# Performance work log

Measured on AMD Instinct MI355X. Metric: run time of the kernel, lower is better.

The kernel has to match this reference:

```python
import jax, jax.numpy as jnp
import numpy as np

N = 100000
E = 1600000
L = 128   # latent_size
H = 128   # hidden_size
O = 128   # output_size


def setup_inputs() -> dict:
    key = jax.random.key(0)
    ks = jax.random.split(key, 16)
    s = 1.0 / np.sqrt(H)
    inp = {
        "z": jax.random.normal(ks[0], (N, L), dtype=jnp.float32),
        "edge_index": jax.random.randint(ks[1], (2, E), 0, N, dtype=jnp.int64),
        # LSTM params (torch order: i, f, g, o)
        "W_ih": jax.random.uniform(ks[2], (4 * H, L), jnp.float32, -s, s),
        "W_hh": jax.random.uniform(ks[3], (4 * H, H), jnp.float32, -s, s),
        "b_ih": jax.random.uniform(ks[4], (4 * H,), jnp.float32, -s, s),
        "b_hh": jax.random.uniform(ks[5], (4 * H,), jnp.float32, -s, s),
        # GCNConv weights (x @ W + b)
        "W1": jax.random.uniform(ks[6], (H, H), jnp.float32, -s, s),
        "b1": jnp.zeros((H,), jnp.float32),
        "W2": jax.random.uniform(ks[7], (H, H), jnp.float32, -s, s),
        "b2": jnp.zeros((H,), jnp.float32),
        # final Linear
        "W3": jax.random.uniform(ks[8], (O, H), jnp.float32, -s, s),
        "b3": jax.random.uniform(ks[9], (O,), jnp.float32, -s, s),
    }
    return inp


def _gcn_conv(x, W, b, src, dst, norm, n_nodes):
    # x: [N, H]; src/dst/norm: [E+N] (self-loops included)
    h = x @ W                                   # [N, H] transform first (H==H)
    msg = h[src] * norm[:, None]                # gather + edge scale
    out = jax.ops.segment_sum(msg, dst, num_segments=n_nodes)  # scatter-add
    return out + b


def _lstm_step(z, W_ih, W_hh, b_ih, b_hh):
    # single time-step, h0 = c0 = 0
    gates = z @ W_ih.T + (jnp.zeros((1, H), z.dtype) @ W_hh.T) + b_ih + b_hh
    i, f, g, o = jnp.split(gates, 4, axis=-1)
    c = jax.nn.sigmoid(i) * jnp.tanh(g)         # f * c0 == 0
    return jax.nn.sigmoid(o) * jnp.tanh(c)


def reference(z, edge_index, W_ih, W_hh, b_ih, b_hh, W1, b1, W2, b2, W3, b3):
    n = z.shape[0]
    # add self-loops (PyG GCNConv default)
    loop = jnp.arange(n, dtype=edge_index.dtype)
    src = jnp.concatenate([edge_index[0], loop])
    dst = jnp.concatenate([edge_index[1], loop])
    # symmetric normalization: deg from dst (incoming, incl. self-loop)
    deg = jax.ops.segment_sum(jnp.ones_like(dst, dtype=z.dtype), dst, num_segments=n)
    dinv = jnp.where(deg > 0, jax.lax.rsqrt(deg), 0.0)
    norm = dinv[src] * dinv[dst]

    h = _lstm_step(z, W_ih, W_hh, b_ih, b_hh)
    x = jax.nn.relu(_gcn_conv(h, W1, b1, src, dst, norm, n))
    x = _gcn_conv(x, W2, b2, src, dst, norm, n)
    return jax.nn.relu(x @ W3.T + b3)
```

## Files before the change

### kernel.cpp

```cpp
#include <hip/hip_runtime.h>
#include <math.h>

typedef __attribute__((ext_vector_type(8))) short short8;
typedef __attribute__((ext_vector_type(4))) float floatx4;

#define HDIM 128
#define NPB 256
#define BKMAX 1024
#define CHUNK 8192
#define STAGE_CAP 8192

__device__ __forceinline__ float bf2f(unsigned short u) {
    unsigned int x = ((unsigned int)u) << 16;
    float f;
    __builtin_memcpy(&f, &x, 4);
    return f;
}
__device__ __forceinline__ unsigned short f2bf(float f) {
    unsigned int x;
    __builtin_memcpy(&x, &f, 4);
    unsigned int r = (x + 0x7fffu + ((x >> 16) & 1u)) >> 16;
    return (unsigned short)r;
}
__device__ __forceinline__ void split1(float v, unsigned short& hi, unsigned short& lo) {
    unsigned int x;
    __builtin_memcpy(&x, &v, 4);
    hi = (unsigned short)(x >> 16);
    lo = f2bf(v - bf2f(hi));
}
__device__ __forceinline__ float fast_sigmoid(float x) {
    return 1.0f / (1.0f + __expf(-x));
}
__device__ __forceinline__ float fast_tanh(float x) {
    float ax = fabsf(x);
    float e = __expf(2.0f * ax);
    float t = 1.0f - 2.0f / (e + 1.0f);
    return copysignf(t, x);
}

__device__ __forceinline__ void gload_lds16(const void* g, void* lds) {
    __builtin_amdgcn_global_load_lds(
        (const __attribute__((address_space(1))) unsigned int*)g,
        (__attribute__((address_space(3))) unsigned int*)lds, 16, 0, 0);
}

__global__ void prep_weights_kernel(const float* __restrict__ Wih,
                                    const float* __restrict__ W1,
                                    const float* __restrict__ W2,
                                    const float* __restrict__ W3,
                                    const float* __restrict__ bih,
                                    const float* __restrict__ bhh,
                                    unsigned short* __restrict__ Wihh, unsigned short* __restrict__ Wihl,
                                    unsigned short* __restrict__ W1h,  unsigned short* __restrict__ W1l,
                                    unsigned short* __restrict__ W2h,  unsigned short* __restrict__ W2l,
                                    unsigned short* __restrict__ W3h,  unsigned short* __restrict__ W3l,
                                    float* __restrict__ bsum) {
    int i = blockIdx.x * 256 + threadIdx.x;
    unsigned short h, l;
    if (i < 65536) {
        split1(Wih[i], h, l);
        Wihh[i] = h; Wihl[i] = l;
    } else if (i < 81920) {
        int t = i - 65536, r = t >> 7, c = t & 127;
        split1(W1[r * HDIM + c], h, l);
        W1h[c * HDIM + r] = h; W1l[c * HDIM + r] = l;
    } else if (i < 98304) {
        int t = i - 81920, r = t >> 7, c = t & 127;
        split1(W2[r * HDIM + c], h, l);
        W2h[c * HDIM + r] = h; W2l[c * HDIM + r] = l;
    } else if (i < 114688) {
        int t = i - 98304;
        split1(W3[t], h, l);
        W3h[t] = h; W3l[t] = l;
    } else if (i < 115200) {
        int t = i - 114688;
        bsum[t] = bih[t] + bhh[t];
    }
}

__global__ __launch_bounds__(256)
void bucket_hist_kernel(const int* __restrict__ ei, int* __restrict__ bcnt,
                        long E, int K) {
    __shared__ int h[BKMAX];
    const int tid = threadIdx.x;
    for (int i = tid; i < K; i += 256) h[i] = 0;
    __syncthreads();
    const long base = (long)blockIdx.x * CHUNK;
#pragma unroll
    for (int j = 0; j < CHUNK / 256; ++j) {
        long e = base + j * 256 + tid;
        if (e < E) atomicAdd(&h[((unsigned)ei[E + e]) >> 8], 1);
    }
    __syncthreads();
    for (int i = tid; i < K; i += 256) {
        int c = h[i];
        if (c) atomicAdd(&bcnt[i], c);
    }
}

__global__ __launch_bounds__(1024)
void scan_buckets_kernel(const int* __restrict__ bcnt, int* __restrict__ gbase,
                         int* __restrict__ gcur, int* __restrict__ offs,
                         int K, int N, int Etot) {
    __shared__ int buf[1024];
    const int t = threadIdx.x;
    const int v = (t < K) ? bcnt[t] : 0;
    buf[t] = v;
    __syncthreads();
    for (int off = 1; off < 1024; off <<= 1) {
        int x = buf[t];
        int y = (t >= off) ? buf[t - off] : 0;
        __syncthreads();
        buf[t] = x + y;
        __syncthreads();
    }
    if (t < K) { gbase[t] = buf[t] - v; gcur[t] = buf[t] - v; }
    if (t == 0) { gbase[K] = Etot; offs[N] = Etot; }
}

__global__ __launch_bounds__(256)
void pair_scatter_kernel(const int* __restrict__ ei, int* __restrict__ gcur,
                         unsigned int* __restrict__ pairs, long E, int K) {
    __shared__ int h[BKMAX];
    __shared__ int cur[BKMAX];
    const int tid = threadIdx.x;
    for (int i = tid; i < K; i += 256) h[i] = 0;
    __syncthreads();
    const long base = (long)blockIdx.x * CHUNK;
#pragma unroll
    for (int j = 0; j < CHUNK / 256; ++j) {
        long e = base + j * 256 + tid;
        if (e < E) atomicAdd(&h[((unsigned)ei[E + e]) >> 8], 1);
    }
    __syncthreads();
    for (int i = tid; i < K; i += 256) {
        int c = h[i];
        cur[i] = c ? atomicAdd(&gcur[i], c) : 0;
    }
    __syncthreads();
#pragma unroll
    for (int j = 0; j < CHUNK / 256; ++j) {
        long e = base + j * 256 + tid;
        if (e < E) {
            unsigned int s = (unsigned int)ei[e];
            unsigned int d = (unsigned int)ei[E + e];
            int b = d >> 8;
            int pos = atomicAdd(&cur[b], 1);
            pairs[pos] = s | ((d & (NPB - 1)) << 24);
        }
    }
}

__global__ __launch_bounds__(256)
void bucket_csr_kernel(const unsigned int* __restrict__ pairs, const int* __restrict__ gbase,
                       int* __restrict__ offs, float* __restrict__ dinv,
                       int* __restrict__ srclist, int N) {
    __shared__ int cnt[NPB];
    __shared__ int red[NPB];
    __shared__ int cur[NPB];
    __shared__ int stage[STAGE_CAP];
    const int tid = threadIdx.x;
    const int b = blockIdx.x;
    const int node0 = b << 8;
    const int nn = min(NPB, N - node0);
    const int ebeg = gbase[b];
    const int eend = gbase[b + 1];
    const int ne = eend - ebeg;

    cnt[tid] = 0;
    __syncthreads();
    for (int i = tid; i < ne; i += 256)
        atomicAdd(&cnt[pairs[ebeg + i] >> 24], 1);
    __syncthreads();
    const int myc = cnt[tid];
    red[tid] = myc;
    __syncthreads();
    for (int off = 1; off < NPB; off <<= 1) {
        int x = red[tid];
        int y = (tid >= off) ? red[tid - off] : 0;
        __syncthreads();
        red[tid] = x + y;
        __syncthreads();
    }
    const int loff = red[tid] - myc;
    if (tid < nn) {
        offs[node0 + tid] = ebeg + loff;
        dinv[node0 + tid] = rsqrtf((float)myc + 1.0f);
    }
    cur[tid] = loff;
    __syncthreads();

    if (ne <= STAGE_CAP) {
        for (int i = tid; i < ne; i += 256) {
            unsigned int p = pairs[ebeg + i];
            int pos = atomicAdd(&cur[p >> 24], 1);
            stage[pos] = (int)(p & 0xFFFFFFu);
        }
        __syncthreads();
        for (int i = tid; i < ne; i += 256)
            srclist[ebeg + i] = stage[i];
    } else {
        for (int i = tid; i < ne; i += 256) {
            unsigned int p = pairs[ebeg + i];
            int pos = atomicAdd(&cur[p >> 24], 1);
            srclist[ebeg + pos] = (int)(p & 0xFFFFFFu);
        }
    }
}

__device__ __forceinline__ void stage_swz(const unsigned short* __restrict__ g,
                                          long rowBase, long maxRow, int kOff,
                                          unsigned short* lds, int nrows, int tid) {
    const int nchunks = nrows << 3;
    for (int L = tid; L < nchunks; L += 256) {
        int r = L >> 3, cS = L & 7;
        int cG = cS ^ (r & 7);
        long gr = rowBase + r;
        if (gr >= maxRow) gr = maxRow - 1;
        gload_lds16(g + gr * HDIM + kOff + cG * 8, lds + (long)L * 8);
    }
}
__device__ __forceinline__ int swz_off(int r, int c0) {
    return (r * 8 + (c0 ^ (r & 7))) * 8;
}

__global__ __launch_bounds__(256, 4)
void gemm_split(const unsigned short* __restrict__ Ah, const unsigned short* __restrict__ Al,
                const unsigned short* __restrict__ Bh, const unsigned short* __restrict__ Bl,
                float* __restrict__ outf, unsigned short* __restrict__ outb, long M,
                const float* __restrict__ rowScale,
                const float* __restrict__ bias, int mode)
{
    __shared__ unsigned short sBh[128 * 64], sBl[128 * 64];
    const int tid = threadIdx.x;
    const long rowBase = (long)blockIdx.x * 64;

    const int wave = tid >> 6;
    const int lane = tid & 63;
    const int quad = lane >> 4;
    const int l16  = lane & 15;
    const int arow = wave * 16 + l16;
    long ag = rowBase + arow;
    if (ag >= M) ag = M - 1;

    short8 rah[2][2], ral[2][2];
#pragma unroll
    for (int h = 0; h < 2; ++h)
#pragma unroll
        for (int kk = 0; kk < 2; ++kk) {
            const long o = ag * HDIM + h * 64 + kk * 32 + quad * 8;
            rah[h][kk] = *(const short8*)(Ah + o);
            ral[h][kk] = *(const short8*)(Al + o);
        }

    floatx4 acc[8];
#pragma unroll
    for (int i = 0; i < 8; ++i) acc[i] = (floatx4)0.0f;

    for (int h = 0; h < 2; ++h) {
        __syncthreads();
        stage_swz(Bh, 0, 128, h * 64, sBh, 128, tid);
        stage_swz(Bl, 0, 128, h * 64, sBl, 128, tid);
        __syncthreads();
#pragma unroll
        for (int kk = 0; kk < 2; ++kk) {
            const int c0 = kk * 4 + quad;
            short8 ah = rah[h][kk];
            short8 al = ral[h][kk];
#pragma unroll
            for (int ct = 0; ct < 8; ++ct) {
                const int bo = swz_off(ct * 16 + l16, c0);
                short8 bh = *(const short8*)(sBh + bo);
                short8 bl = *(const short8*)(sBl + bo);
                acc[ct] = __builtin_amdgcn_mfma_f32_16x16x32_bf16(ah, bh, acc[ct], 0, 0, 0);
                acc[ct] = __builtin_amdgcn_mfma_f32_16x16x32_bf16(ah, bl, acc[ct], 0, 0, 0);
                acc[ct] = __builtin_amdgcn_mfma_f32_16x16x32_bf16(al, bh, acc[ct], 0, 0, 0);
            }
        }
    }

#pragma unroll
    for (int ct = 0; ct < 8; ++ct) {
#pragma unroll
        for (int r = 0; r < 4; ++r) {
            long m = rowBase + wave * 16 + quad * 4 + r;
            if (m < M) {
                int n = ct * 16 + l16;
                float v = acc[ct][r];
                if (mode == 0) {
                    v *= rowScale[m];
                    outb[m * HDIM + n] = f2bf(v);
                } else {
                    v += bias[n];
                    v = fmaxf(v, 0.0f);
                    outf[m * HDIM + n] = v;
                }
            }
        }
    }
}

__global__ __launch_bounds__(384, 3)
void lstm_gemm_split(const float* __restrict__ Z,
                     const unsigned short* __restrict__ Wh, const unsigned short* __restrict__ Wl,
                     const float* __restrict__ bsum,
                     unsigned short* __restrict__ Hh, unsigned short* __restrict__ Hl, long M)
{
    __shared__ unsigned short sBh[2][128 * 64], sBl[2][128 * 64];
    const int tid = threadIdx.x;
    const long rowBase = (long)blockIdx.x * 96;

    const int wave = tid >> 6;
    const int lane = tid & 63;
    const int quad = lane >> 4;
    const int l16  = lane & 15;
    const int arow = wave * 16 + l16;
    long ag = rowBase + arow;
    if (ag >= M) ag = M - 1;

    short8 rah[2][2], ral[2][2];
#pragma unroll
    for (int h = 0; h < 2; ++h)
#pragma unroll
        for (int kk = 0; kk < 2; ++kk) {
            const float* p = Z + ag * HDIM + h * 64 + kk * 32 + quad * 8;
            float4 f0 = *(const float4*)p;
            float4 f1 = *(const float4*)(p + 4);
            float f[8] = {f0.x, f0.y, f0.z, f0.w, f1.x, f1.y, f1.z, f1.w};
#pragma unroll
            for (int e = 0; e < 8; ++e) {
                unsigned short hi, lo;
                split1(f[e], hi, lo);
                rah[h][kk][e] = (short)hi;
                ral[h][kk][e] = (short)lo;
            }
        }

    const int stager = (tid < 256);

    auto stage_phase = [&](int ph, int b) {
        if (!stager) return;
        const int g = ph >> 1, h = ph & 1;
        const int gateRow = (g == 0) ? 0 : ((g == 1) ? 256 : 384);
        const unsigned short* gh = Wh + (long)gateRow * HDIM + h * 64;
        const unsigned short* gl = Wl + (long)gateRow * HDIM + h * 64;
#pragma unroll
        for (int it = 0; it < 4; ++it) {
            int L = it * 256 + tid;
            int r = L >> 3, cS = L & 7, cG = cS ^ (r & 7);
            gload_lds16(gh + (long)r * HDIM + cG * 8, &sBh[b][L * 8]);
        }
#pragma unroll
        for (int it = 0; it < 4; ++it) {
            int L = it * 256 + tid;
            int r = L >> 3, cS = L & 7, cG = cS ^ (r & 7);
            gload_lds16(gl + (long)r * HDIM + cG * 8, &sBl[b][L * 8]);
        }
    };

    floatx4 acc[8];
    floatx4 st[8];
#pragma unroll
    for (int i = 0; i < 8; ++i) acc[i] = (floatx4)0.0f;

    stage_phase(0, 0);

#pragma unroll
    for (int ph = 0; ph < 6; ++ph) {
        const int b = ph & 1;
        if (ph < 5) stage_phase(ph + 1, b ^ 1);
        if (ph == 2) {
#pragma unroll
            for (int ct = 0; ct < 8; ++ct) {
                const float bb = bsum[ct * 16 + l16];
#pragma unroll
                for (int r = 0; r < 4; ++r)
                    st[ct][r] = fast_sigmoid(acc[ct][r] + bb);
                acc[ct] = (floatx4)0.0f;
            }
        } else if (ph == 4) {
#pragma unroll
            for (int ct = 0; ct < 8; ++ct) {
                const float bb = bsum[256 + ct * 16 + l16];
#pragma unroll
                for (int r = 0; r < 4; ++r) {
                    float cv = st[ct][r] * fast_tanh(acc[ct][r] + bb);
                    st[ct][r] = fast_tanh(cv);
                }
                acc[ct] = (floatx4)0.0f;
            }
        }
        if (ph < 5) asm volatile("s_waitcnt vmcnt(8)" ::: "memory");
        else        asm volatile("s_waitcnt vmcnt(0)" ::: "memory");
        __builtin_amdgcn_s_barrier();
        asm volatile("" ::: "memory");
        const int hh_ = ph & 1;
#pragma unroll
        for (int kk = 0; kk < 2; ++kk) {
            const int c0 = kk * 4 + quad;
            short8 a_h = rah[hh_][kk];
            short8 a_l = ral[hh_][kk];
#pragma unroll
            for (int ct = 0; ct < 8; ++ct) {
                const int bo = swz_off(ct * 16 + l16, c0);
                short8 bh = *(const short8*)(&sBh[b][0] + bo);
                short8 bl = *(const short8*)(&sBl[b][0] + bo);
                acc[ct] = __builtin_amdgcn_mfma_f32_16x16x32_bf16(a_h, bh, acc[ct], 0, 0, 0);
                acc[ct] = __builtin_amdgcn_mfma_f32_16x16x32_bf16(a_h, bl, acc[ct], 0, 0, 0);
                acc[ct] = __builtin_amdgcn_mfma_f32_16x16x32_bf16(a_l, bh, acc[ct], 0, 0, 0);
            }
        }
        asm volatile("s_waitcnt lgkmcnt(0)" ::: "memory");
        __builtin_amdgcn_s_barrier();
        asm volatile("" ::: "memory");
    }

#pragma unroll
    for (int ct = 0; ct < 8; ++ct) {
        const float bb = bsum[384 + ct * 16 + l16];
#pragma unroll
        for (int r = 0; r < 4; ++r) {
            long m = rowBase + wave * 16 + quad * 4 + r;
            if (m < M) {
                float hv = fast_sigmoid(acc[ct][r] + bb) * st[ct][r];
                unsigned short hh, hl;
                split1(hv, hh, hl);
                int n = ct * 16 + l16;
                Hh[m * HDIM + n] = hh;
                Hl[m * HDIM + n] = hl;
            }
        }
    }
}

__global__ __launch_bounds__(256, 4)
void aggregate_kernel(const unsigned short* __restrict__ t, const int* __restrict__ srclist,
                      const int* __restrict__ offs, const float* __restrict__ dinv,
                      const float* __restrict__ bias, int doRelu,
                      unsigned short* __restrict__ Xh, unsigned short* __restrict__ Xl, long N)
{
    long node = (long)blockIdx.x * 4 + (threadIdx.x >> 6);
    if (node >= N) return;
    const int lane = threadIdx.x & 63;
    const int c = lane * 2;
    const int beg = offs[node];
    const int end = offs[node + 1];
    float s0[8], s1[8];
#pragma unroll
    for (int q = 0; q < 8; ++q) { s0[q] = 0.0f; s1[q] = 0.0f; }
    int j = beg;
    for (; j + 8 <= end; j += 8) {
        int srcs[8];
#pragma unroll
        for (int q = 0; q < 8; ++q) srcs[q] = srclist[j + q];
        unsigned int p[8];
#pragma unroll
        for (int q = 0; q < 8; ++q) p[q] = *(const unsigned int*)(t + (long)srcs[q] * HDIM + c);
#pragma unroll
        for (int q = 0; q < 8; ++q) {
            s0[q] += bf2f((unsigned short)(p[q] & 0xffffu));
            s1[q] += bf2f((unsigned short)(p[q] >> 16));
        }
    }
    for (; j + 4 <= end; j += 4) {
        int srcs[4];
#pragma unroll
        for (int q = 0; q < 4; ++q) srcs[q] = srclist[j + q];
#pragma unroll
        for (int q = 0; q < 4; ++q) {
            unsigned int p = *(const unsigned int*)(t + (long)srcs[q] * HDIM + c);
            s0[q] += bf2f((unsigned short)(p & 0xffffu));
            s1[q] += bf2f((unsigned short)(p >> 16));
        }
    }
    for (; j < end; ++j) {
        unsigned int p = *(const unsigned int*)(t + (long)srclist[j] * HDIM + c);
        s0[0] += bf2f((unsigned short)(p & 0xffffu));
        s1[0] += bf2f((unsigned short)(p >> 16));
    }
    const unsigned int ps = *(const unsigned int*)(t + node * HDIM + c);
    s0[0] += bf2f((unsigned short)(ps & 0xffffu));
    s1[0] += bf2f((unsigned short)(ps >> 16));
    float a0 = ((s0[0] + s0[1]) + (s0[2] + s0[3])) + ((s0[4] + s0[5]) + (s0[6] + s0[7]));
    float a1 = ((s1[0] + s1[1]) + (s1[2] + s1[3])) + ((s1[4] + s1[5]) + (s1[6] + s1[7]));
    const float d = dinv[node];
    float v0 = d * a0 + bias[c];
    float v1 = d * a1 + bias[c + 1];
    if (doRelu) { v0 = fmaxf(v0, 0.0f); v1 = fmaxf(v1, 0.0f); }
    unsigned short h0, l0, h1, l1;
    split1(v0, h0, l0);
    split1(v1, h1, l1);
    *(unsigned int*)(Xh + node * HDIM + c) = (unsigned int)h0 | ((unsigned int)h1 << 16);
    *(unsigned int*)(Xl + node * HDIM + c) = (unsigned int)l0 | ((unsigned int)l1 << 16);
}

extern "C" void kernel_launch(void* const* d_in, const int* in_sizes, int n_in,
                              void* d_out, int out_size, void* d_ws, size_t ws_size,
                              hipStream_t stream)
{
    const float* z   = (const float*)d_in[0];
    const int*   ei  = (const int*)d_in[1];
    const float* Wih = (const float*)d_in[2];
    const float* bih = (const float*)d_in[4];
    const float* bhh = (const float*)d_in[5];
    const float* W1  = (const float*)d_in[6];
    const float* b1  = (const float*)d_in[7];
    const float* W2  = (const float*)d_in[8];
    const float* b2  = (const float*)d_in[9];
    const float* W3  = (const float*)d_in[10];
    const float* b3  = (const float*)d_in[11];
    float* out = (float*)d_out;

    const long N = in_sizes[0] / HDIM;
    const long E = in_sizes[1] / 2;
    const int  K = (int)((N + NPB - 1) / NPB);

    char* ws = (char*)d_ws;
    size_t off = 0;
    auto alloc = [&](size_t bytes) {
        char* p = ws + off;
        off += (bytes + 255) & ~(size_t)255;
        return (void*)p;
    };
    int*   bcnt    = (int*)alloc(K * 4);
    int*   gbase   = (int*)alloc((K + 1) * 4);
    int*   gcur    = (int*)alloc(K * 4);
    int*   offs    = (int*)alloc((N + 1) * 4);
    float* dinv    = (float*)alloc(N * 4);
    unsigned int* pairs = (unsigned int*)alloc(E * 4);
    int*   srclist = (int*)alloc(E * 4);
    unsigned short* P1h = (unsigned short*)alloc(N * HDIM * 2);
    unsigned short* P1l = (unsigned short*)alloc(N * HDIM * 2);
    unsigned short* P2h = (unsigned short*)alloc(N * HDIM * 2);
    unsigned short* P2l = (unsigned short*)alloc(N * HDIM * 2);
    unsigned short* Tb  = (unsigned short*)alloc(N * HDIM * 2);
    unsigned short* Wihh = (unsigned short*)alloc(512 * HDIM * 2);
    unsigned short* Wihl = (unsigned short*)alloc(512 * HDIM * 2);
    unsigned short* W1h  = (unsigned short*)alloc(HDIM * HDIM * 2);
    unsigned short* W1l  = (unsigned short*)alloc(HDIM * HDIM * 2);
    unsigned short* W2h  = (unsigned short*)alloc(HDIM * HDIM * 2);
    unsigned short* W2l  = (unsigned short*)alloc(HDIM * HDIM * 2);
    unsigned short* W3h  = (unsigned short*)alloc(HDIM * HDIM * 2);
    unsigned short* W3l  = (unsigned short*)alloc(HDIM * HDIM * 2);
    float* bsum = (float*)alloc(512 * 4);

    const int gblocks  = (int)((N + 63) / 64);
    const int lblocks  = (int)((N + 95) / 96);
    const int ablocks  = (int)((N + 3) / 4);
    const int cblocks  = (int)((E + CHUNK - 1) / CHUNK);

    hipMemsetAsync(bcnt, 0, K * 4, stream);
    bucket_hist_kernel<<<cblocks, 256, 0, stream>>>(ei, bcnt, E, K);
    scan_buckets_kernel<<<1, 1024, 0, stream>>>(bcnt, gbase, gcur, offs, K, (int)N, (int)E);
    pair_scatter_kernel<<<cblocks, 256, 0, stream>>>(ei, gcur, pairs, E, K);
    bucket_csr_kernel<<<K, 256, 0, stream>>>(pairs, gbase, offs, dinv, srclist, (int)N);

    prep_weights_kernel<<<451, 256, 0, stream>>>(Wih, W1, W2, W3, bih, bhh,
                                                 Wihh, Wihl, W1h, W1l, W2h, W2l, W3h, W3l, bsum);

    lstm_gemm_split<<<lblocks, 384, 0, stream>>>(z, Wihh, Wihl, bsum, P2h, P2l, N);

    gemm_split<<<gblocks, 256, 0, stream>>>(P2h, P2l, W1h, W1l, nullptr, Tb, N, dinv, nullptr, 0);
    aggregate_kernel<<<ablocks, 256, 0, stream>>>(Tb, srclist, offs, dinv, b1, 1, P1h, P1l, N);

    gemm_split<<<gblocks, 256, 0, stream>>>(P1h, P1l, W2h, W2l, nullptr, Tb, N, dinv, nullptr, 0);
    aggregate_kernel<<<ablocks, 256, 0, stream>>>(Tb, srclist, offs, dinv, b2, 0, P2h, P2l, N);

    gemm_split<<<gblocks, 256, 0, stream>>>(P2h, P2l, W3h, W3l, out, nullptr, N, nullptr, b3, 1);
}
```

Baseline: 486.3 us.

## Stage full high-part LSTM weights in LDS once, read low part from global

Measured after the change: 561.3 us. +15.4%, slower.

```diff
diff --git a/kernel.cpp b/kernel.cpp
--- a/kernel.cpp
+++ b/kernel.cpp
@@ -300,15 +300,15 @@
     }
 }
 
-__global__ __launch_bounds__(384, 3)
+__global__ __launch_bounds__(768, 3)
 void lstm_gemm_split(const float* __restrict__ Z,
                      const unsigned short* __restrict__ Wh, const unsigned short* __restrict__ Wl,
                      const float* __restrict__ bsum,
                      unsigned short* __restrict__ Hh, unsigned short* __restrict__ Hl, long M)
 {
-    __shared__ unsigned short sBh[2][128 * 64], sBl[2][128 * 64];
+    __shared__ unsigned short sBh[3 * 128 * 128];
     const int tid = threadIdx.x;
-    const long rowBase = (long)blockIdx.x * 96;
+    const long rowBase = (long)blockIdx.x * 192;
 
     const int wave = tid >> 6;
     const int lane = tid & 63;
@@ -318,6 +318,17 @@
     long ag = rowBase + arow;
     if (ag >= M) ag = M - 1;
 
+#pragma unroll
+    for (int it = 0; it < 8; ++it) {
+        int L = it * 768 + tid;
+        int gate = L >> 11;
+        int rem  = L & 2047;
+        int r = rem >> 4, cS = rem & 15;
+        int cG = (cS & 8) | ((cS ^ r) & 7);
+        int gRow = (gate == 0) ? 0 : ((gate == 1) ? 256 : 384);
+        gload_lds16(Wh + (long)(gRow + r) * HDIM + cG * 8, &sBh[(long)L * 8]);
+    }
+
     short8 rah[2][2], ral[2][2];
 #pragma unroll
     for (int h = 0; h < 2; ++h)
@@ -336,40 +347,19 @@
             }
         }
 
-    const int stager = (tid < 256);
-
-    auto stage_phase = [&](int ph, int b) {
-        if (!stager) return;
-        const int g = ph >> 1, h = ph & 1;
-        const int gateRow = (g == 0) ? 0 : ((g == 1) ? 256 : 384);
-        const unsigned short* gh = Wh + (long)gateRow * HDIM + h * 64;
-        const unsigned short* gl = Wl + (long)gateRow * HDIM + h * 64;
-#pragma unroll
-        for (int it = 0; it < 4; ++it) {
-            int L = it * 256 + tid;
-            int r = L >> 3, cS = L & 7, cG = cS ^ (r & 7);
-            gload_lds16(gh + (long)r * HDIM + cG * 8, &sBh[b][L * 8]);
-        }
-#pragma unroll
-        for (int it = 0; it < 4; ++it) {
-            int L = it * 256 + tid;
-            int r = L >> 3, cS = L & 7, cG = cS ^ (r & 7);
-            gload_lds16(gl + (long)r * HDIM + cG * 8, &sBl[b][L * 8]);
-        }
-    };
+    __syncthreads();
 
     floatx4 acc[8];
     floatx4 st[8];
 #pragma unroll
     for (int i = 0; i < 8; ++i) acc[i] = (floatx4)0.0f;
 
-    stage_phase(0, 0);
-
-#pragma unroll
-    for (int ph = 0; ph < 6; ++ph) {
-        const int b = ph & 1;
-        if (ph < 5) stage_phase(ph + 1, b ^ 1);
-        if (ph == 2) {
+#pragma unroll
+    for (int gate = 0; gate < 3; ++gate) {
+        const int gRow = (gate == 0) ? 0 : ((gate == 1) ? 256 : 384);
+        const unsigned short* gl = Wl + (long)gRow * HDIM;
+        const int gBase = gate << 11;
+        if (gate == 1) {
 #pragma unroll
             for (int ct = 0; ct < 8; ++ct) {
                 const float bb = bsum[ct * 16 + l16];
@@ -378,7 +368,7 @@
                     st[ct][r] = fast_sigmoid(acc[ct][r] + bb);
                 acc[ct] = (floatx4)0.0f;
             }
-        } else if (ph == 4) {
+        } else if (gate == 2) {
 #pragma unroll
             for (int ct = 0; ct < 8; ++ct) {
                 const float bb = bsum[256 + ct * 16 + l16];
@@ -390,29 +380,22 @@
                 acc[ct] = (floatx4)0.0f;
             }
         }
-        if (ph < 5) asm volatile("s_waitcnt vmcnt(8)" ::: "memory");
-        else        asm volatile("s_waitcnt vmcnt(0)" ::: "memory");
-        __builtin_amdgcn_s_barrier();
-        asm volatile("" ::: "memory");
-        const int hh_ = ph & 1;
-#pragma unroll
-        for (int kk = 0; kk < 2; ++kk) {
-            const int c0 = kk * 4 + quad;
-            short8 a_h = rah[hh_][kk];
-            short8 a_l = ral[hh_][kk];
+#pragma unroll
+        for (int ks = 0; ks < 4; ++ks) {
+            short8 a_h = rah[ks >> 1][ks & 1];
+            short8 a_l = ral[ks >> 1][ks & 1];
 #pragma unroll
             for (int ct = 0; ct < 8; ++ct) {
-                const int bo = swz_off(ct * 16 + l16, c0);
-                short8 bh = *(const short8*)(&sBh[b][0] + bo);
-                short8 bl = *(const short8*)(&sBl[b][0] + bo);
+                const int r = ct * 16 + l16;
+                const int c = ks * 4 + quad;
+                const int slot = (c & 8) | ((c ^ r) & 7);
+                short8 bh = *(const short8*)(&sBh[(long)(gBase + (r << 4) + slot) * 8]);
+                short8 bl = *(const short8*)(gl + (long)r * HDIM + ks * 32 + quad * 8);
                 acc[ct] = __builtin_amdgcn_mfma_f32_16x16x32_bf16(a_h, bh, acc[ct], 0, 0, 0);
                 acc[ct] = __builtin_amdgcn_mfma_f32_16x16x32_bf16(a_h, bl, acc[ct], 0, 0, 0);
                 acc[ct] = __builtin_amdgcn_mfma_f32_16x16x32_bf16(a_l, bh, acc[ct], 0, 0, 0);
             }
         }
-        asm volatile("s_waitcnt lgkmcnt(0)" ::: "memory");
-        __builtin_amdgcn_s_barrier();
-        asm volatile("" ::: "memory");
     }
 
 #pragma unroll
@@ -545,7 +528,7 @@
     float* bsum = (float*)alloc(512 * 4);
 
     const int gblocks  = (int)((N + 63) / 64);
-    const int lblocks  = (int)((N + 95) / 96);
+    const int lblocks  = (int)((N + 191) / 192);
     const int ablocks  = (int)((N + 3) / 4);
     const int cblocks  = (int)((E + CHUNK - 1) / CHUNK);
 
@@ -558,7 +541,7 @@
     prep_weights_kernel<<<451, 256, 0, stream>>>(Wih, W1, W2, W3, bih, bhh,
                                                  Wihh, Wihl, W1h, W1l, W2h, W2l, W3h, W3l, bsum);
 
-    lstm_gemm_split<<<lblocks, 384, 0, stream>>>(z, Wihh, Wihl, bsum, P2h, P2l, N);
+    lstm_gemm_split<<<lblocks, 768, 0, stream>>>(z, Wihh, Wihl, bsum, P2h, P2l, N);
 
     gemm_split<<<gblocks, 256, 0, stream>>>(P2h, P2l, W1h, W1l, nullptr, Tb, N, dinv, nullptr, 0);
     aggregate_kernel<<<ablocks, 256, 0, stream>>>(Tb, srclist, offs, dinv, b1, 1, P1h, P1l, N);
```
